# Kernel optimization log

Hardware: AMD Instinct MI355X
Metric: run time of the kernel (lower is better)

## Reference

```python
import jax, jax.numpy as jnp
import numpy as np
from jax import lax

B, H, W, C = 64, 224, 224, 3
FLAT = 27040  # 52*52*10 after localization convs/pools


def conv_relu(x, w, b):
    y = lax.conv_general_dilated(x, w, (1, 1), 'VALID',
                                 dimension_numbers=('NHWC', 'HWIO', 'NHWC'))
    return jax.nn.relu(y + b)


def maxpool2(x):
    return lax.reduce_window(x, -jnp.inf, lax.max, (1, 2, 2, 1), (1, 2, 2, 1), 'VALID')


def affine_grid(h, w, theta):
    # normalized coords in [-1, 1]
    xt, yt = jnp.meshgrid(jnp.linspace(-1.0, 1.0, w), jnp.linspace(-1.0, 1.0, h))
    grid = jnp.stack([xt.ravel(), yt.ravel(), jnp.ones(h * w, theta.dtype)], 0)  # (3, h*w)
    g = jnp.einsum('bij,jp->bip', theta, grid)  # (B, 2, h*w)
    return g.reshape(-1, 2, h, w)


def bilinear_sampler(img, xs, ys):
    # xs, ys: (B, h, w) in [-1, 1]; img: (B, H, W, C)
    max_y, max_x = img.shape[1] - 1, img.shape[2] - 1
    x = 0.5 * (xs + 1.0) * max_x
    y = 0.5 * (ys + 1.0) * max_y
    x0 = jnp.clip(jnp.floor(x).astype(jnp.int32), 0, max_x)
    x1 = jnp.clip(x0 + 1, 0, max_x)
    y0 = jnp.clip(jnp.floor(y).astype(jnp.int32), 0, max_y)
    y1 = jnp.clip(y0 + 1, 0, max_y)
    b = jnp.arange(img.shape[0])[:, None, None]
    Ia = img[b, y0, x0]  # (B,h,w,C)
    Ib = img[b, y1, x0]
    Ic = img[b, y0, x1]
    Id = img[b, y1, x1]
    x0f, x1f = x0.astype(x.dtype), x1.astype(x.dtype)
    y0f, y1f = y0.astype(y.dtype), y1.astype(y.dtype)
    wa = ((x1f - x) * (y1f - y))[..., None]
    wb = ((x1f - x) * (y - y0f))[..., None]
    wc = ((x - x0f) * (y1f - y))[..., None]
    wd = ((x - x0f) * (y - y0f))[..., None]
    return wa * Ia + wb * Ib + wc * Ic + wd * Id


def setup_inputs() -> dict:
    key = jax.random.key(0)
    ks = jax.random.split(key, 6)
    inputs = jax.random.normal(ks[0], (B, H, W, C), jnp.float32)
    conv1_w = jax.random.normal(ks[1], (7, 7, 3, 8), jnp.float32) * (2.0 / (7 * 7 * 3)) ** 0.5
    conv1_b = jnp.zeros((8,), jnp.float32)
    conv2_w = jax.random.normal(ks[2], (5, 5, 8, 10), jnp.float32) * (2.0 / (5 * 5 * 8)) ** 0.5
    conv2_b = jnp.zeros((10,), jnp.float32)
    fc1_w = jax.random.normal(ks[3], (FLAT, 32), jnp.float32) * (2.0 / FLAT) ** 0.5
    fc1_b = jnp.zeros((32,), jnp.float32)
    fc2_w = jax.random.normal(ks[4], (32, 6), jnp.float32) * 0.01
    fc2_b = jnp.array([1, 0, 0, 0, 1, 0], jnp.float32)  # identity affine init
    return dict(inputs=inputs, conv1_w=conv1_w, conv1_b=conv1_b,
                conv2_w=conv2_w, conv2_b=conv2_b, fc1_w=fc1_w, fc1_b=fc1_b,
                fc2_w=fc2_w, fc2_b=fc2_b)


def reference(inputs, conv1_w, conv1_b, conv2_w, conv2_b, fc1_w, fc1_b, fc2_w, fc2_b):
    xs = maxpool2(conv_relu(inputs, conv1_w, conv1_b))
    xs = maxpool2(conv_relu(xs, conv2_w, conv2_b))
    xs = xs.reshape(xs.shape[0], -1)  # (B, 27040)
    h1 = jax.nn.relu(xs @ fc1_w + fc1_b)
    theta = (h1 @ fc2_w + fc2_b).reshape(-1, 2, 3)
    grid = affine_grid(H, W, theta)  # (B, 2, H, W)
    return bilinear_sampler(inputs, grid[:, 0], grid[:, 1])
```

## Files before the change

### kernel.cpp

```cpp
#include <hip/hip_runtime.h>


__global__ __launch_bounds__(256) void k_conv1(
    const float* __restrict__ in, const float* __restrict__ w,
    const float* __restrict__ bias, double* __restrict__ out) {
  __shared__ float win[10 * 672];
  __shared__ double sw[147 * 8];
  __shared__ double sb[8];
  for (int i = threadIdx.x; i < 1176; i += 256) sw[i] = (double)w[i];
  if (threadIdx.x < 8) sb[threadIdx.x] = (double)bias[threadIdx.x];

  int g = blockIdx.x & 7;
  int i = blockIdx.x >> 3;
  int b = g * 8 + i / 55;
  int tile = i % 55;
  int r0 = 4 * tile;

  const float* ib = in + (size_t)b * 224 * 672 / 3 * 3;
  {
    const float* ibb = in + (size_t)b * 150528;
    for (int idx = threadIdx.x; idx < 10 * 168; idx += 256) {
      int rr = idx / 168, c4 = idx % 168;
      int row = min(r0 + rr, 223);
      float4 v = reinterpret_cast<const float4*>(ibb + (size_t)row * 672)[c4];
      reinterpret_cast<float4*>(&win[rr * 672])[c4] = v;
    }
  }
  __syncthreads();

  int pix = threadIdx.x;
  if (pix < 218) {
    int px = pix % 109;
    int pyl = pix / 109;
    int py = 2 * tile + pyl;
    if (py < 109) {
      double acc[2][2][8];
#pragma unroll
      for (int ii = 0; ii < 2; ++ii)
#pragma unroll
        for (int j = 0; j < 2; ++j)
#pragma unroll
          for (int k = 0; k < 8; ++k) acc[ii][j][k] = 0.0;

      for (int ky = 0; ky < 7; ++ky) {
        const float* r0p = &win[(2 * pyl + ky) * 672 + 6 * px];
        const float* r1p = r0p + 672;
        float a0[24], a1[24];
#pragma unroll
        for (int j = 0; j < 12; ++j) {
          float2 u = reinterpret_cast<const float2*>(r0p)[j];
          a0[2 * j] = u.x; a0[2 * j + 1] = u.y;
          float2 v = reinterpret_cast<const float2*>(r1p)[j];
          a1[2 * j] = v.x; a1[2 * j + 1] = v.y;
        }
#pragma unroll
        for (int kx = 0; kx < 7; ++kx) {
#pragma unroll
          for (int c = 0; c < 3; ++c) {
            double v00 = (double)a0[kx * 3 + c];
            double v01 = (double)a0[kx * 3 + 3 + c];
            double v10 = (double)a1[kx * 3 + c];
            double v11 = (double)a1[kx * 3 + 3 + c];
            const double* wp = &sw[((ky * 7 + kx) * 3 + c) * 8];
#pragma unroll
            for (int oc = 0; oc < 8; ++oc) {
              double wv = wp[oc];
              acc[0][0][oc] = fma(v00, wv, acc[0][0][oc]);
              acc[0][1][oc] = fma(v01, wv, acc[0][1][oc]);
              acc[1][0][oc] = fma(v10, wv, acc[1][0][oc]);
              acc[1][1][oc] = fma(v11, wv, acc[1][1][oc]);
            }
          }
        }
      }

      double* op = out + ((size_t)b * 11881 + (size_t)py * 109 + px) * 8;
#pragma unroll
      for (int oc = 0; oc < 8; ++oc) {
        double m = fmax(fmax(acc[0][0][oc], acc[0][1][oc]),
                        fmax(acc[1][0][oc], acc[1][1][oc]));
        op[oc] = fmax(m + sb[oc], 0.0);
      }
    }
  }
}

__global__ __launch_bounds__(256) void k_conv2(
    const double* __restrict__ in, const float* __restrict__ w,
    const float* __restrict__ bias, double* __restrict__ out) {
  __shared__ double win[8 * 109 * 4];
  __shared__ double sw[200 * 12];
  __shared__ double sb[10];
  for (int i = threadIdx.x; i < 2000; i += 256) {
    int tap = i / 10, oc = i % 10;
    sw[tap * 12 + (oc / 5) * 6 + (oc % 5)] = (double)w[i];
  }
  if (threadIdx.x < 10) sb[threadIdx.x] = (double)bias[threadIdx.x];

  int g = blockIdx.x & 7;
  int i = blockIdx.x >> 3;
  int b = g * 8 + i / 26;
  int tile = i % 26;
  int r0 = 4 * tile;

  int px = threadIdx.x % 52;
  int pyl = (threadIdx.x / 52) & 1;
  int oh = threadIdx.x / 104;

  double acc[2][2][5];
#pragma unroll
  for (int ii = 0; ii < 2; ++ii)
#pragma unroll
    for (int jj = 0; jj < 2; ++jj)
#pragma unroll
      for (int k = 0; k < 5; ++k) acc[ii][jj][k] = 0.0;

  const double* ib = in + (size_t)b * 11881 * 8;

  for (int h = 0; h < 2; ++h) {
    __syncthreads();
    for (int idx = threadIdx.x; idx < 1744; idx += 256) {
      int d2 = idx & 1;
      int x = (idx >> 1) % 109;
      int rr = (idx >> 1) / 109;
      double2 v = *reinterpret_cast<const double2*>(
          ib + ((size_t)(r0 + rr) * 109 + x) * 8 + h * 4 + d2 * 2);
      *reinterpret_cast<double2*>(&win[((size_t)rr * 109 + x) * 4 + d2 * 2]) = v;
    }
    __syncthreads();

    if (threadIdx.x < 208) {
#pragma unroll
      for (int ky = 0; ky < 5; ++ky) {
        int rr0 = 2 * pyl + ky;
#pragma unroll
        for (int kx = 0; kx < 5; ++kx) {
          const double* p00 = &win[((size_t)rr0 * 109 + 2 * px + kx) * 4];
          const double* p01 = p00 + 4;
          const double* p10 = p00 + 109 * 4;
          const double* p11 = p10 + 4;
#pragma unroll
          for (int cc = 0; cc < 4; ++cc) {
            int c = h * 4 + cc;
            double v00 = p00[cc], v01 = p01[cc];
            double v10 = p10[cc], v11 = p11[cc];
            const double* wp = &sw[((ky * 5 + kx) * 8 + c) * 12 + oh * 6];
#pragma unroll
            for (int oc = 0; oc < 5; ++oc) {
              double wv = wp[oc];
              acc[0][0][oc] = fma(v00, wv, acc[0][0][oc]);
              acc[0][1][oc] = fma(v01, wv, acc[0][1][oc]);
              acc[1][0][oc] = fma(v10, wv, acc[1][0][oc]);
              acc[1][1][oc] = fma(v11, wv, acc[1][1][oc]);
            }
          }
        }
      }
    }
  }

  if (threadIdx.x < 208) {
    int py = 2 * tile + pyl;
    double* op = out + ((size_t)b * 2704 + (size_t)py * 52 + px) * 10 + oh * 5;
#pragma unroll
    for (int oc = 0; oc < 5; ++oc) {
      double m = fmax(fmax(acc[0][0][oc], acc[0][1][oc]),
                      fmax(acc[1][0][oc], acc[1][1][oc]));
      op[oc] = fmax(m + sb[oh * 5 + oc], 0.0);
    }
  }
}

__global__ __launch_bounds__(256) void k_fc1(
    const double* __restrict__ xs, const float* __restrict__ w1,
    double* __restrict__ part) {
  int b = blockIdx.x >> 3;
  int q = blockIdx.x & 7;
  int oc = threadIdx.x & 31;
  int s = threadIdx.x >> 5;
  const double* xrow = xs + (size_t)b * 27040;

  int i0 = q * 3392 + s * 424;
  int i1 = min(i0 + 424, 27040);
  double s0 = 0.0, s1 = 0.0;
  for (int i = i0; i + 1 < i1; i += 2) {
    s0 = fma(xrow[i],     (double)w1[(size_t)i * 32 + oc],       s0);
    s1 = fma(xrow[i + 1], (double)w1[(size_t)(i + 1) * 32 + oc], s1);
  }
  if (((i1 - i0) & 1) && i0 < i1)
    s0 = fma(xrow[i1 - 1], (double)w1[(size_t)(i1 - 1) * 32 + oc], s0);

  __shared__ double red[8][32];
  red[s][oc] = s0 + s1;
  __syncthreads();
  if (threadIdx.x < 32) {
    double v = 0.0;
#pragma unroll
    for (int k = 0; k < 8; ++k) v += red[k][threadIdx.x];
    part[((size_t)b * 8 + q) * 32 + threadIdx.x] = v;
  }
}

__global__ __launch_bounds__(64) void k_fc2(
    const double* __restrict__ part, const float* __restrict__ b1,
    const float* __restrict__ w2, const float* __restrict__ b2,
    double* __restrict__ theta) {
  int b = blockIdx.x;
  __shared__ double h1[32];
  if (threadIdx.x < 32) {
    double v = (double)b1[threadIdx.x];
#pragma unroll
    for (int q = 0; q < 8; ++q) v += part[((size_t)b * 8 + q) * 32 + threadIdx.x];
    h1[threadIdx.x] = v > 0.0 ? v : 0.0;
  }
  __syncthreads();
  if (threadIdx.x < 6) {
    double v = (double)b2[threadIdx.x];
#pragma unroll
    for (int k = 0; k < 32; ++k) v += h1[k] * (double)w2[k * 6 + threadIdx.x];
    theta[b * 6 + threadIdx.x] = v;
  }
}

__global__ __launch_bounds__(256) void k_sample(
    const float* __restrict__ img, const double* __restrict__ theta,
    float* __restrict__ out) {
  int idx = blockIdx.x * 256 + threadIdx.x;
  if (idx >= 64 * 224 * 224) return;
  int x = idx % 224;
  int t = idx / 224;
  int y = t % 224;
  int b = t / 224;

  const double* th = theta + b * 6;
  double t0 = th[0], t1 = th[1], t2 = th[2];
  double t3 = th[3], t4 = th[4], t5 = th[5];

  double xn = -1.0 + x * (2.0 / 223.0);
  double yn = -1.0 + y * (2.0 / 223.0);
  double xf = 0.5 * (t0 * xn + t1 * yn + t2 + 1.0) * 223.0;
  double yf = 0.5 * (t3 * xn + t4 * yn + t5 + 1.0) * 223.0;

  int x0 = (int)floor(xf);
  int y0 = (int)floor(yf);
  x0 = min(max(x0, 0), 223);
  y0 = min(max(y0, 0), 223);
  int x1 = min(x0 + 1, 223);
  int y1 = min(y0 + 1, 223);

  double x0f = (double)x0, x1f = (double)x1;
  double y0f = (double)y0, y1f = (double)y1;
  double wa = (x1f - xf) * (y1f - yf);
  double wb = (x1f - xf) * (yf - y0f);
  double wc = (xf - x0f) * (y1f - yf);
  double wd = (xf - x0f) * (yf - y0f);

  const float* p = img + (size_t)b * 150528;
  const float* Ia = p + ((size_t)y0 * 224 + x0) * 3;
  const float* Ib = p + ((size_t)y1 * 224 + x0) * 3;
  const float* Ic = p + ((size_t)y0 * 224 + x1) * 3;
  const float* Id = p + ((size_t)y1 * 224 + x1) * 3;

  float* op = out + (size_t)idx * 3;
#pragma unroll
  for (int c = 0; c < 3; ++c) {
    op[c] = (float)(wa * (double)Ia[c] + wb * (double)Ib[c] +
                    wc * (double)Ic[c] + wd * (double)Id[c]);
  }
}

extern "C" void kernel_launch(void* const* d_in, const int* in_sizes, int n_in,
                              void* d_out, int out_size, void* d_ws, size_t ws_size,
                              hipStream_t stream) {
  const float* inputs  = (const float*)d_in[0];
  const float* conv1_w = (const float*)d_in[1];
  const float* conv1_b = (const float*)d_in[2];
  const float* conv2_w = (const float*)d_in[3];
  const float* conv2_b = (const float*)d_in[4];
  const float* fc1_w   = (const float*)d_in[5];
  const float* fc1_b   = (const float*)d_in[6];
  const float* fc2_w   = (const float*)d_in[7];
  const float* fc2_b   = (const float*)d_in[8];
  float* outp = (float*)d_out;

  double* theta = (double*)d_ws;
  double* part  = (double*)((char*)d_ws + 4096);
  double* pool1 = (double*)((char*)d_ws + 4096 + 131072);
  double* pool2 = pool1 + 6081152;

  k_conv1<<<55 * 64, 256, 0, stream>>>(inputs, conv1_w, conv1_b, pool1);
  k_conv2<<<26 * 64, 256, 0, stream>>>(pool1, conv2_w, conv2_b, pool2);
  k_fc1<<<512, 256, 0, stream>>>(pool2, fc1_w, part);
  k_fc2<<<64, 64, 0, stream>>>(part, fc1_b, fc2_w, fc2_b, theta);
  k_sample<<<(64 * 224 * 224 + 255) / 256, 256, 0, stream>>>(inputs, theta, outp);
}
```

Before: 476.5 us.

## Pack conv output pixels linearly per block so all threads do work

Both conv kernels now map each block's 256 threads onto a contiguous run of flattened output pixels, replacing the fixed row-pair tiles that left 38 (conv1) or 48 (conv2) threads idle. The input window grows to cover the rows a run spans, which means more shared memory and redundant global loads per block. Conv2 also moves its shared window to a channel-planar layout with padded rows, aiming for cheaper and less bank-conflicted reads. Grid sizes shrink to match.

```diff
diff --git a/kernel.cpp b/kernel.cpp
--- a/kernel.cpp
+++ b/kernel.cpp
@@ -4,7 +4,7 @@
 __global__ __launch_bounds__(256) void k_conv1(
     const float* __restrict__ in, const float* __restrict__ w,
     const float* __restrict__ bias, double* __restrict__ out) {
-  __shared__ float win[10 * 672];
+  __shared__ float win[14 * 672];
   __shared__ double sw[147 * 8];
   __shared__ double sb[8];
   for (int i = threadIdx.x; i < 1176; i += 256) sw[i] = (double)w[i];
@@ -12,14 +12,15 @@
 
   int g = blockIdx.x & 7;
   int i = blockIdx.x >> 3;
-  int b = g * 8 + i / 55;
-  int tile = i % 55;
-  int r0 = 4 * tile;
-
-  const float* ib = in + (size_t)b * 224 * 672 / 3 * 3;
+  int b = g * 8 + i / 47;
+  int tile = i % 47;
+  int p0 = tile * 256;
+  int py0 = p0 / 109;
+  int r0 = 2 * py0;
+
   {
     const float* ibb = in + (size_t)b * 150528;
-    for (int idx = threadIdx.x; idx < 10 * 168; idx += 256) {
+    for (int idx = threadIdx.x; idx < 14 * 168; idx += 256) {
       int rr = idx / 168, c4 = idx % 168;
       int row = min(r0 + rr, 223);
       float4 v = reinterpret_cast<const float4*>(ibb + (size_t)row * 672)[c4];
@@ -28,59 +29,58 @@
   }
   __syncthreads();
 
-  int pix = threadIdx.x;
-  if (pix < 218) {
+  int pix = p0 + threadIdx.x;
+  if (pix < 11881) {
     int px = pix % 109;
-    int pyl = pix / 109;
-    int py = 2 * tile + pyl;
-    if (py < 109) {
-      double acc[2][2][8];
-#pragma unroll
-      for (int ii = 0; ii < 2; ++ii)
-#pragma unroll
-        for (int j = 0; j < 2; ++j)
-#pragma unroll
-          for (int k = 0; k < 8; ++k) acc[ii][j][k] = 0.0;
-
-      for (int ky = 0; ky < 7; ++ky) {
-        const float* r0p = &win[(2 * pyl + ky) * 672 + 6 * px];
-        const float* r1p = r0p + 672;
-        float a0[24], a1[24];
-#pragma unroll
-        for (int j = 0; j < 12; ++j) {
-          float2 u = reinterpret_cast<const float2*>(r0p)[j];
-          a0[2 * j] = u.x; a0[2 * j + 1] = u.y;
-          float2 v = reinterpret_cast<const float2*>(r1p)[j];
-          a1[2 * j] = v.x; a1[2 * j + 1] = v.y;
-        }
-#pragma unroll
-        for (int kx = 0; kx < 7; ++kx) {
-#pragma unroll
-          for (int c = 0; c < 3; ++c) {
-            double v00 = (double)a0[kx * 3 + c];
-            double v01 = (double)a0[kx * 3 + 3 + c];
-            double v10 = (double)a1[kx * 3 + c];
-            double v11 = (double)a1[kx * 3 + 3 + c];
-            const double* wp = &sw[((ky * 7 + kx) * 3 + c) * 8];
-#pragma unroll
-            for (int oc = 0; oc < 8; ++oc) {
-              double wv = wp[oc];
-              acc[0][0][oc] = fma(v00, wv, acc[0][0][oc]);
-              acc[0][1][oc] = fma(v01, wv, acc[0][1][oc]);
-              acc[1][0][oc] = fma(v10, wv, acc[1][0][oc]);
-              acc[1][1][oc] = fma(v11, wv, acc[1][1][oc]);
-            }
+    int py = pix / 109;
+    int lrb = 2 * py - r0;
+
+    double acc[2][2][8];
+#pragma unroll
+    for (int ii = 0; ii < 2; ++ii)
+#pragma unroll
+      for (int j = 0; j < 2; ++j)
+#pragma unroll
+        for (int k = 0; k < 8; ++k) acc[ii][j][k] = 0.0;
+
+    for (int ky = 0; ky < 7; ++ky) {
+      const float* r0p = &win[(lrb + ky) * 672 + 6 * px];
+      const float* r1p = r0p + 672;
+      float a0[24], a1[24];
+#pragma unroll
+      for (int j = 0; j < 12; ++j) {
+        float2 u = reinterpret_cast<const float2*>(r0p)[j];
+        a0[2 * j] = u.x; a0[2 * j + 1] = u.y;
+        float2 v = reinterpret_cast<const float2*>(r1p)[j];
+        a1[2 * j] = v.x; a1[2 * j + 1] = v.y;
+      }
+#pragma unroll
+      for (int kx = 0; kx < 7; ++kx) {
+#pragma unroll
+        for (int c = 0; c < 3; ++c) {
+          double v00 = (double)a0[kx * 3 + c];
+          double v01 = (double)a0[kx * 3 + 3 + c];
+          double v10 = (double)a1[kx * 3 + c];
+          double v11 = (double)a1[kx * 3 + 3 + c];
+          const double* wp = &sw[((ky * 7 + kx) * 3 + c) * 8];
+#pragma unroll
+          for (int oc = 0; oc < 8; ++oc) {
+            double wv = wp[oc];
+            acc[0][0][oc] = fma(v00, wv, acc[0][0][oc]);
+            acc[0][1][oc] = fma(v01, wv, acc[0][1][oc]);
+            acc[1][0][oc] = fma(v10, wv, acc[1][0][oc]);
+            acc[1][1][oc] = fma(v11, wv, acc[1][1][oc]);
           }
         }
       }
-
-      double* op = out + ((size_t)b * 11881 + (size_t)py * 109 + px) * 8;
-#pragma unroll
-      for (int oc = 0; oc < 8; ++oc) {
-        double m = fmax(fmax(acc[0][0][oc], acc[0][1][oc]),
-                        fmax(acc[1][0][oc], acc[1][1][oc]));
-        op[oc] = fmax(m + sb[oc], 0.0);
-      }
+    }
+
+    double* op = out + ((size_t)b * 11881 + pix) * 8;
+#pragma unroll
+    for (int oc = 0; oc < 8; ++oc) {
+      double m = fmax(fmax(acc[0][0][oc], acc[0][1][oc]),
+                      fmax(acc[1][0][oc], acc[1][1][oc]));
+      op[oc] = fmax(m + sb[oc], 0.0);
     }
   }
 }
@@ -88,7 +88,7 @@
 __global__ __launch_bounds__(256) void k_conv2(
     const double* __restrict__ in, const float* __restrict__ w,
     const float* __restrict__ bias, double* __restrict__ out) {
-  __shared__ double win[8 * 109 * 4];
+  __shared__ double win2[4 * 12 * 112];
   __shared__ double sw[200 * 12];
   __shared__ double sb[10];
   for (int i = threadIdx.x; i < 2000; i += 256) {
@@ -99,13 +99,19 @@
 
   int g = blockIdx.x & 7;
   int i = blockIdx.x >> 3;
-  int b = g * 8 + i / 26;
-  int tile = i % 26;
-  int r0 = 4 * tile;
-
-  int px = threadIdx.x % 52;
-  int pyl = (threadIdx.x / 52) & 1;
-  int oh = threadIdx.x / 104;
+  int b = g * 8 + i / 22;
+  int tile = i % 22;
+  int wi = tile * 256 + threadIdx.x;
+  bool valid = wi < 5408;
+  int oh = wi & 1;
+  int pix = wi >> 1;
+  int p0 = tile * 128;
+  int py0 = p0 / 52;
+  int r0 = 2 * py0;
+
+  int px = pix % 52;
+  int py = pix / 52;
+  int lrb = 2 * py - r0;
 
   double acc[2][2][5];
 #pragma unroll
@@ -119,31 +125,33 @@
 
   for (int h = 0; h < 2; ++h) {
     __syncthreads();
-    for (int idx = threadIdx.x; idx < 1744; idx += 256) {
+    for (int idx = threadIdx.x; idx < 12 * 109 * 2; idx += 256) {
       int d2 = idx & 1;
-      int x = (idx >> 1) % 109;
+      int x  = (idx >> 1) % 109;
       int rr = (idx >> 1) / 109;
+      int row = min(r0 + rr, 108);
       double2 v = *reinterpret_cast<const double2*>(
-          ib + ((size_t)(r0 + rr) * 109 + x) * 8 + h * 4 + d2 * 2);
-      *reinterpret_cast<double2*>(&win[((size_t)rr * 109 + x) * 4 + d2 * 2]) = v;
+          ib + ((size_t)row * 109 + x) * 8 + h * 4 + d2 * 2);
+      win2[((d2 * 2) * 12 + rr) * 112 + x] = v.x;
+      win2[((d2 * 2 + 1) * 12 + rr) * 112 + x] = v.y;
     }
     __syncthreads();
 
-    if (threadIdx.x < 208) {
+    if (valid) {
 #pragma unroll
       for (int ky = 0; ky < 5; ++ky) {
-        int rr0 = 2 * pyl + ky;
+        int rr0 = lrb + ky;
 #pragma unroll
         for (int kx = 0; kx < 5; ++kx) {
-          const double* p00 = &win[((size_t)rr0 * 109 + 2 * px + kx) * 4];
-          const double* p01 = p00 + 4;
-          const double* p10 = p00 + 109 * 4;
-          const double* p11 = p10 + 4;
+          int xx = 2 * px + kx;
 #pragma unroll
           for (int cc = 0; cc < 4; ++cc) {
             int c = h * 4 + cc;
-            double v00 = p00[cc], v01 = p01[cc];
-            double v10 = p10[cc], v11 = p11[cc];
+            const double* pbase = &win2[(cc * 12 + rr0) * 112 + xx];
+            double v00 = pbase[0];
+            double v01 = pbase[1];
+            double v10 = pbase[112];
+            double v11 = pbase[113];
             const double* wp = &sw[((ky * 5 + kx) * 8 + c) * 12 + oh * 6];
 #pragma unroll
             for (int oc = 0; oc < 5; ++oc) {
@@ -159,9 +167,8 @@
     }
   }
 
-  if (threadIdx.x < 208) {
-    int py = 2 * tile + pyl;
-    double* op = out + ((size_t)b * 2704 + (size_t)py * 52 + px) * 10 + oh * 5;
+  if (valid) {
+    double* op = out + ((size_t)b * 2704 + pix) * 10 + oh * 5;
 #pragma unroll
     for (int oc = 0; oc < 5; ++oc) {
       double m = fmax(fmax(acc[0][0][oc], acc[0][1][oc]),
@@ -288,8 +295,8 @@
   double* pool1 = (double*)((char*)d_ws + 4096 + 131072);
   double* pool2 = pool1 + 6081152;
 
-  k_conv1<<<55 * 64, 256, 0, stream>>>(inputs, conv1_w, conv1_b, pool1);
-  k_conv2<<<26 * 64, 256, 0, stream>>>(pool1, conv2_w, conv2_b, pool2);
+  k_conv1<<<47 * 64, 256, 0, stream>>>(inputs, conv1_w, conv1_b, pool1);
+  k_conv2<<<22 * 64, 256, 0, stream>>>(pool1, conv2_w, conv2_b, pool2);
   k_fc1<<<512, 256, 0, stream>>>(pool2, fc1_w, part);
   k_fc2<<<64, 64, 0, stream>>>(part, fc1_b, fc2_w, fc2_b, theta);
   k_sample<<<(64 * 224 * 224 + 255) / 256, 256, 0, stream>>>(inputs, theta, outp);
```

Measured after the change: 428.7 us. 1.11x faster.
